# Performance work log

Hardware: AMD Instinct MI355X
Metric: run time of the kernel (lower is better)

Reference implementation:

```python
import jax, jax.numpy as jnp
import numpy as np

MASKED = True


def setup_inputs() -> dict:
    key = jax.random.key(0)
    kq, kk, kv = jax.random.split(key, 3)
    shape = (4, 16, 2048, 64)  # [B, H, S, d]
    q = jax.random.normal(kq, shape, dtype=jnp.float32)
    k = jax.random.normal(kk, shape, dtype=jnp.float32)
    v = jax.random.normal(kv, shape, dtype=jnp.float32)
    return {"q": q, "k": k, "v": v}


def reference(q, k, v):
    d = k.shape[-1]
    scale = 1.0 / jnp.sqrt(jnp.asarray(d, dtype=q.dtype))
    # [B, H, S, S]
    att = jnp.einsum("bhqd,bhkd->bhqk", q, k) * scale
    if MASKED:
        # Faithful to torch source: tril of the scores, then mask where zero
        tri = jnp.tril(att)
        att = jnp.where(tri == 0, -jnp.inf, att)
    att = jax.nn.softmax(att, axis=-1)
    return jnp.einsum("bhqk,bhkd->bhqd", att, v)
```

## Files before the change

kernel.cpp:

```cpp
#include <hip/hip_runtime.h>
#include <hip/hip_bf16.h>

typedef __attribute__((ext_vector_type(8)))  short bf16x8;
typedef __attribute__((ext_vector_type(4)))  float f32x4;
typedef __attribute__((ext_vector_type(16))) float f32x16;
typedef unsigned short ushort_t;

#define S_LEN 2048
#define D_DIM 64

#if __has_builtin(__builtin_amdgcn_exp2f)
#define EXP2(x) __builtin_amdgcn_exp2f(x)
#else
#define EXP2(x) __expf((x) * 0.6931471805599453f)
#endif

__device__ __forceinline__ short f2bf(float f) {
  union { float f; unsigned u; } x; x.f = f;
  unsigned r = x.u + 0x7fffu + ((x.u >> 16) & 1u);
  return (short)(r >> 16);
}

__device__ __forceinline__ unsigned cvtpk_bf16(float lo, float hi) {
  unsigned r;
  asm("v_cvt_pk_bf16_f32 %0, %1, %2" : "=v"(r) : "v"(lo), "v"(hi));
  return r;
}

__device__ __forceinline__ void pl32swap(unsigned& a, unsigned& b) {
  asm volatile("v_permlane32_swap_b32 %0, %1" : "+v"(a), "+v"(b));
}

__device__ __forceinline__ void gl_lds16(const ushort_t* g, ushort_t* l) {
  __builtin_amdgcn_global_load_lds(
      (const __attribute__((address_space(1))) unsigned*)g,
      (__attribute__((address_space(3))) unsigned*)l, 16, 0, 0);
}

__global__ void conv_bf16_kernel(const float* __restrict__ in,
                                 ushort_t* __restrict__ out, long n8) {
  long i = (long)blockIdx.x * blockDim.x + threadIdx.x;
  const long stride = (long)gridDim.x * blockDim.x;
  for (; i < n8; i += stride) {
    const float4* p = (const float4*)(in + i * 8);
    float4 a = p[0], b = p[1];
    bf16x8 t;
    t[0]=f2bf(a.x); t[1]=f2bf(a.y); t[2]=f2bf(a.z); t[3]=f2bf(a.w);
    t[4]=f2bf(b.x); t[5]=f2bf(b.y); t[6]=f2bf(b.z); t[7]=f2bf(b.w);
    *(bf16x8*)(out + i * 8) = t;
  }
}

__global__ void transpose_v_kernel(const float* __restrict__ V,
                                   ushort_t* __restrict__ Vt) {
  const int h  = blockIdx.x >> 5;
  const int s0 = (blockIdx.x & 31) * 64;
  const float* Vh = V + (size_t)h * S_LEN * D_DIM;
  ushort_t* Vth   = Vt + (size_t)h * D_DIM * S_LEN;
  __shared__ float tile[64][65];
  const int r  = threadIdx.x >> 2;
  const int c4 = (threadIdx.x & 3) * 16;
#pragma unroll
  for (int j = 0; j < 16; j += 4) {
    float4 x = *(const float4*)(Vh + (size_t)(s0 + r) * D_DIM + c4 + j);
    tile[r][c4 + j + 0] = x.x; tile[r][c4 + j + 1] = x.y;
    tile[r][c4 + j + 2] = x.z; tile[r][c4 + j + 3] = x.w;
  }
  __syncthreads();
  bf16x8 o0, o1;
#pragma unroll
  for (int j = 0; j < 8; ++j) o0[j] = f2bf(tile[c4 + j][r]);
#pragma unroll
  for (int j = 0; j < 8; ++j) o1[j] = f2bf(tile[c4 + 8 + j][r]);
  *(bf16x8*)(Vth + (size_t)r * S_LEN + s0 + c4)     = o0;
  *(bf16x8*)(Vth + (size_t)r * S_LEN + s0 + c4 + 8) = o1;
}

__global__ __launch_bounds__(256, 4)
void flash32_kernel(const float* __restrict__ Qf, const ushort_t* __restrict__ Kb,
                    const ushort_t* __restrict__ Vt, float* __restrict__ Og) {
  const int tid = threadIdx.x;
  const int l   = tid & 63;
  const int wv  = tid >> 6;
  const int hi  = l >> 5;
  const int l31 = l & 31;
  const int l7  = l & 7;
  const int l8  = l >> 3;

  const int qperm[16] = {15,14,13,12, 0,1,2,3, 11,10,9,8, 4,5,6,7};
  const int bid  = blockIdx.x;
  const int head = bid & 63;
  const int qidx = qperm[bid >> 6];
  const int q0   = qidx * 128;
  const int nt   = 2 * qidx + 2;

  const float*    Qh = Qf + (size_t)head * S_LEN * D_DIM;
  const ushort_t* Kh = Kb + (size_t)head * S_LEN * D_DIM;
  const ushort_t* Vh = Vt + (size_t)head * D_DIM * S_LEN;
  float*          Oh = Og + (size_t)head * S_LEN * D_DIM;

  __shared__ ushort_t smK[2][64 * 64];
  __shared__ ushort_t smV[2][64 * 64];

  const int qrow  = q0 + wv * 32 + l31;
  const int qminw = q0 + wv * 32;
  const int qmaxw = qminw + 31;

  const int swsrc = (l7 ^ l8) * 8;

#define STAGE(T, B) do {                                                   \
    const int kv_ = (T) * 64;                                              \
    _Pragma("unroll")                                                      \
    for (int u_ = 0; u_ < 4; ++u_) {                                       \
      const int idx_ = wv * 4 + u_;                                        \
      if (idx_ < 8) {                                                      \
        const int row_ = idx_ * 8 + l8;                                    \
        gl_lds16(Kh + (size_t)(kv_ + row_) * 64 + swsrc,                   \
                 &smK[B][idx_ * 512]);                                     \
      } else {                                                             \
        const int d_ = (idx_ - 8) * 8 + l8;                                \
        gl_lds16(Vh + (size_t)d_ * S_LEN + kv_ + swsrc,                    \
                 &smV[B][(idx_ - 8) * 512]);                               \
      }                                                                    \
    }                                                                      \
  } while (0)

  STAGE(0, 0);

  bf16x8 qf[4];
  {
    const float sc = 0.125f * 1.44269504089f;
    const float* qp = Qh + (size_t)qrow * D_DIM + 8 * hi;
#pragma unroll
    for (int ks = 0; ks < 4; ++ks) {
      float4 x = *(const float4*)(qp + ks * 16);
      float4 y = *(const float4*)(qp + ks * 16 + 4);
      bf16x8 t;
      t[0]=f2bf(x.x*sc); t[1]=f2bf(x.y*sc);
      t[2]=f2bf(x.z*sc); t[3]=f2bf(x.w*sc);
      t[4]=f2bf(y.x*sc); t[5]=f2bf(y.y*sc);
      t[6]=f2bf(y.z*sc); t[7]=f2bf(y.w*sc);
      qf[ks] = t;
    }
  }

  f32x16 accA, accB;
#pragma unroll
  for (int i = 0; i < 16; ++i) { accA[i] = 0.f; accB[i] = 0.f; }
  float m_run = -1e30f, l_run = 0.f;

  for (int t = 0; t < nt; ++t) {
    const int kv0 = t * 64;
    if (t + 1 < nt) {
      STAGE(t + 1, (t + 1) & 1);
      asm volatile("s_waitcnt vmcnt(4)" ::: "memory");
    } else {
      asm volatile("s_waitcnt vmcnt(0)" ::: "memory");
    }
    __builtin_amdgcn_s_barrier();
    __builtin_amdgcn_sched_barrier(0);

    if (kv0 <= qmaxw) {
      const ushort_t* kb = smK[t & 1];
      const ushort_t* vb = smV[t & 1];
      const int rb = l31 * 64;

      f32x16 s0, s1;
#pragma unroll
      for (int i = 0; i < 16; ++i) { s0[i] = 0.f; s1[i] = 0.f; }
      __builtin_amdgcn_s_setprio(1);
#pragma unroll
      for (int ks = 0; ks < 4; ++ks) {
        const int ch = ((ks * 2 + hi) ^ l7) * 8;
        bf16x8 a0 = *(const bf16x8*)(kb + rb + ch);
        bf16x8 a1 = *(const bf16x8*)(kb + 2048 + rb + ch);
        s0 = __builtin_amdgcn_mfma_f32_32x32x16_bf16(a0, qf[ks], s0, 0, 0, 0);
        s1 = __builtin_amdgcn_mfma_f32_32x32x16_bf16(a1, qf[ks], s1, 0, 0, 0);
      }
      __builtin_amdgcn_s_setprio(0);

      if (kv0 + 63 > qminw) {
#pragma unroll
        for (int r = 0; r < 16; ++r) {
          const int crow = (r & 3) + 8 * (r >> 2) + 4 * hi;
          if (kv0 + crow > qrow)      s0[r] = -INFINITY;
          if (kv0 + 32 + crow > qrow) s1[r] = -INFINITY;
        }
      }

      float a8[8];
#pragma unroll
      for (int i = 0; i < 8; ++i)
        a8[i] = fmaxf(fmaxf(s0[i], s0[i + 8]), fmaxf(s1[i], s1[i + 8]));
#pragma unroll
      for (int i = 0; i < 4; ++i) a8[i] = fmaxf(a8[i], a8[i + 4]);
      float mx = fmaxf(fmaxf(a8[0], a8[2]), fmaxf(a8[1], a8[3]));
      mx = fmaxf(mx, __shfl_xor(mx, 32, 64));

      if (!__all(mx - m_run <= 11.0f)) {
        const float mn    = fmaxf(m_run, mx);
        const float alpha = EXP2(m_run - mn);
        m_run = mn;
        l_run *= alpha;
        accA *= alpha;
        accB *= alpha;
      }

#pragma unroll
      for (int i = 0; i < 16; ++i) s0[i] = EXP2(s0[i] - m_run);
#pragma unroll
      for (int i = 0; i < 16; ++i) s1[i] = EXP2(s1[i] - m_run);
      float b8[8];
#pragma unroll
      for (int i = 0; i < 8; ++i)
        b8[i] = (s0[i] + s0[i + 8]) + (s1[i] + s1[i + 8]);
#pragma unroll
      for (int i = 0; i < 4; ++i) b8[i] += b8[i + 4];
      float sum = (b8[0] + b8[2]) + (b8[1] + b8[3]);
      sum += __shfl_xor(sum, 32, 64);
      l_run += sum;

      bf16x8 pw[4];
#pragma unroll
      for (int ks = 0; ks < 4; ++ks) {
        const int r0 = (ks & 1) * 8;
        unsigned w0, w1, w2, w3;
        if (ks < 2) {
          w0 = cvtpk_bf16(s0[r0+0], s0[r0+1]); w2 = cvtpk_bf16(s0[r0+4], s0[r0+5]);
          w1 = cvtpk_bf16(s0[r0+2], s0[r0+3]); w3 = cvtpk_bf16(s0[r0+6], s0[r0+7]);
        } else {
          w0 = cvtpk_bf16(s1[r0+0], s1[r0+1]); w2 = cvtpk_bf16(s1[r0+4], s1[r0+5]);
          w1 = cvtpk_bf16(s1[r0+2], s1[r0+3]); w3 = cvtpk_bf16(s1[r0+6], s1[r0+7]);
        }
        pl32swap(w0, w2);
        pl32swap(w1, w3);
        union { unsigned u[4]; bf16x8 v; } pu;
        pu.u[0] = w0; pu.u[1] = w1; pu.u[2] = w2; pu.u[3] = w3;
        pw[ks] = pu.v;
      }

      __builtin_amdgcn_s_setprio(1);
#pragma unroll
      for (int ks = 0; ks < 4; ++ks) {
        const int ch = ((ks * 2 + hi) ^ l7) * 8;
        bf16x8 va = *(const bf16x8*)(vb + rb + ch);
        bf16x8 vB = *(const bf16x8*)(vb + 2048 + rb + ch);
        accA = __builtin_amdgcn_mfma_f32_32x32x16_bf16(va, pw[ks], accA, 0, 0, 0);
        accB = __builtin_amdgcn_mfma_f32_32x32x16_bf16(vB, pw[ks], accB, 0, 0, 0);
      }
      __builtin_amdgcn_s_setprio(0);
    }
    __builtin_amdgcn_s_barrier();
  }
#undef STAGE

  const float inv = 1.0f / l_run;
  float* op = Oh + (size_t)qrow * D_DIM + 4 * hi;
#pragma unroll
  for (int m4 = 0; m4 < 4; ++m4) {
    float4 a = { accA[4*m4+0]*inv, accA[4*m4+1]*inv,
                 accA[4*m4+2]*inv, accA[4*m4+3]*inv };
    *(float4*)(op + 8 * m4) = a;
    float4 b = { accB[4*m4+0]*inv, accB[4*m4+1]*inv,
                 accB[4*m4+2]*inv, accB[4*m4+3]*inv };
    *(float4*)(op + 32 + 8 * m4) = b;
  }
}

#define BQ 64
#define BK 64
#define LDK 72
#define LDP 72

__device__ __forceinline__ unsigned pack_bf(float lo, float hi) {
  return (unsigned)(unsigned short)f2bf(lo) |
         ((unsigned)(unsigned short)f2bf(hi) << 16);
}

__global__ __launch_bounds__(256, 2)
void flash_fwd_kernel(const float* __restrict__ Qg, const float* __restrict__ Kg,
                      const float* __restrict__ Vg, float* __restrict__ Og) {
  const int tid  = threadIdx.x;
  const int lane = tid & 63;
  const int wv   = tid >> 6;
  const int grp  = lane >> 4;
  const int l16  = lane & 15;
  const int bid = blockIdx.x;
  const int qb  = 31 - (bid & 31);
  const int bh  = bid >> 5;
  const int q0  = qb * BQ;
  const size_t hoff = (size_t)bh * S_LEN * D_DIM;
  const float* Qh = Qg + hoff;
  const float* Kh = Kg + hoff;
  const float* Vh = Vg + hoff;
  float*       Oh = Og + hoff;
  __shared__ short sK [BK][LDK];
  __shared__ short sVT[D_DIM][LDP];
  __shared__ short sP [4][16][LDP];
  bf16x8 qf[2];
  {
    const float* qrow = Qh + (size_t)(q0 + wv*16 + l16) * D_DIM + grp*8;
#pragma unroll
    for (int kc = 0; kc < 2; ++kc) {
      float4 a = *reinterpret_cast<const float4*>(qrow + kc*32);
      float4 b = *reinterpret_cast<const float4*>(qrow + kc*32 + 4);
      bf16x8 t;
      t[0]=f2bf(a.x*0.125f); t[1]=f2bf(a.y*0.125f);
      t[2]=f2bf(a.z*0.125f); t[3]=f2bf(a.w*0.125f);
      t[4]=f2bf(b.x*0.125f); t[5]=f2bf(b.y*0.125f);
      t[6]=f2bf(b.z*0.125f); t[7]=f2bf(b.w*0.125f);
      qf[kc] = t;
    }
  }
  f32x4 acc[4];
#pragma unroll
  for (int nb = 0; nb < 4; ++nb) acc[nb] = (f32x4){0.f, 0.f, 0.f, 0.f};
  float m_i[4] = {-INFINITY, -INFINITY, -INFINITY, -INFINITY};
  float l_i[4] = {0.f, 0.f, 0.f, 0.f};
  const int srow = tid >> 2;
  const int scb  = tid & 3;
  for (int kt = 0; kt <= qb; ++kt) {
    const int kv0 = kt * BK;
    __syncthreads();
    {
      const float* src = Kh + (size_t)(kv0 + srow) * D_DIM + scb*16;
      float4 x0 = *reinterpret_cast<const float4*>(src);
      float4 x1 = *reinterpret_cast<const float4*>(src + 4);
      float4 x2 = *reinterpret_cast<const float4*>(src + 8);
      float4 x3 = *reinterpret_cast<const float4*>(src + 12);
      bf16x8 lo, hi;
      lo[0]=f2bf(x0.x); lo[1]=f2bf(x0.y); lo[2]=f2bf(x0.z); lo[3]=f2bf(x0.w);
      lo[4]=f2bf(x1.x); lo[5]=f2bf(x1.y); lo[6]=f2bf(x1.z); lo[7]=f2bf(x1.w);
      hi[0]=f2bf(x2.x); hi[1]=f2bf(x2.y); hi[2]=f2bf(x2.z); hi[3]=f2bf(x2.w);
      hi[4]=f2bf(x3.x); hi[5]=f2bf(x3.y); hi[6]=f2bf(x3.z); hi[7]=f2bf(x3.w);
      *reinterpret_cast<bf16x8*>(&sK[srow][scb*16])     = lo;
      *reinterpret_cast<bf16x8*>(&sK[srow][scb*16 + 8]) = hi;
    }
    {
      const float* src = Vh + (size_t)(kv0 + scb*16) * D_DIM + srow;
      bf16x8 lo, hi;
#pragma unroll
      for (int j = 0; j < 8; ++j) lo[j] = f2bf(src[(size_t)j * D_DIM]);
#pragma unroll
      for (int j = 0; j < 8; ++j) hi[j] = f2bf(src[(size_t)(j + 8) * D_DIM]);
      *reinterpret_cast<bf16x8*>(&sVT[srow][scb*16])     = lo;
      *reinterpret_cast<bf16x8*>(&sVT[srow][scb*16 + 8]) = hi;
    }
    __syncthreads();
    f32x4 sc[4];
#pragma unroll
    for (int nb = 0; nb < 4; ++nb) {
      f32x4 c = (f32x4){0.f, 0.f, 0.f, 0.f};
#pragma unroll
      for (int kc = 0; kc < 2; ++kc) {
        bf16x8 kf = *reinterpret_cast<const bf16x8*>(&sK[nb*16 + l16][kc*32 + grp*8]);
        c = __builtin_amdgcn_mfma_f32_16x16x32_bf16(qf[kc], kf, c, 0, 0, 0);
      }
      sc[nb] = c;
    }
    const bool diag = (kt == qb);
#pragma unroll
    for (int r = 0; r < 4; ++r) {
      const int qi = wv*16 + grp*4 + r;
      float s0 = sc[0][r], s1 = sc[1][r], s2 = sc[2][r], s3 = sc[3][r];
      if (diag) {
        if (l16 +  0 > qi) s0 = -INFINITY;
        if (l16 + 16 > qi) s1 = -INFINITY;
        if (l16 + 32 > qi) s2 = -INFINITY;
        if (l16 + 48 > qi) s3 = -INFINITY;
      }
      float mx = fmaxf(fmaxf(s0, s1), fmaxf(s2, s3));
#pragma unroll
      for (int off = 8; off; off >>= 1)
        mx = fmaxf(mx, __shfl_xor(mx, off, 64));
      const float mn    = fmaxf(m_i[r], mx);
      const float alpha = __expf(m_i[r] - mn);
      const float p0 = __expf(s0 - mn);
      const float p1 = __expf(s1 - mn);
      const float p2 = __expf(s2 - mn);
      const float p3 = __expf(s3 - mn);
      float rs = (p0 + p1) + (p2 + p3);
#pragma unroll
      for (int off = 8; off; off >>= 1)
        rs += __shfl_xor(rs, off, 64);
      l_i[r] = l_i[r] * alpha + rs;
      m_i[r] = mn;
      acc[0][r] *= alpha; acc[1][r] *= alpha;
      acc[2][r] *= alpha; acc[3][r] *= alpha;
      const float n0 = __shfl_xor(p0, 1, 64);
      const float n1 = __shfl_xor(p1, 1, 64);
      const float n2 = __shfl_xor(p2, 1, 64);
      const float n3 = __shfl_xor(p3, 1, 64);
      if (!(lane & 1)) {
        const int prow = grp*4 + r;
        unsigned* base = reinterpret_cast<unsigned*>(&sP[wv][prow][l16]);
        base[0]  = pack_bf(p0, n0);
        base[8]  = pack_bf(p1, n1);
        base[16] = pack_bf(p2, n2);
        base[24] = pack_bf(p3, n3);
      }
    }
    bf16x8 pf[2];
#pragma unroll
    for (int kc = 0; kc < 2; ++kc)
      pf[kc] = *reinterpret_cast<const bf16x8*>(&sP[wv][l16][kc*32 + grp*8]);
#pragma unroll
    for (int nb = 0; nb < 4; ++nb) {
#pragma unroll
      for (int kc = 0; kc < 2; ++kc) {
        bf16x8 vf = *reinterpret_cast<const bf16x8*>(&sVT[l16 + 16*nb][kc*32 + grp*8]);
        acc[nb] = __builtin_amdgcn_mfma_f32_16x16x32_bf16(pf[kc], vf, acc[nb], 0, 0, 0);
      }
    }
  }
#pragma unroll
  for (int r = 0; r < 4; ++r) {
    const float inv = 1.0f / l_i[r];
    float* orow = Oh + (size_t)(q0 + wv*16 + grp*4 + r) * D_DIM + l16;
#pragma unroll
    for (int nb = 0; nb < 4; ++nb)
      orow[nb*16] = acc[nb][r] * inv;
  }
}

extern "C" void kernel_launch(void* const* d_in, const int* in_sizes, int n_in,
                              void* d_out, int out_size, void* d_ws, size_t ws_size,
                              hipStream_t stream) {
  (void)n_in; (void)out_size;
  const float* q = (const float*)d_in[0];
  const float* k = (const float*)d_in[1];
  const float* v = (const float*)d_in[2];
  float* o = (float*)d_out;
  const int bh = in_sizes[0] / (S_LEN * D_DIM);
  const size_t elems = (size_t)bh * S_LEN * D_DIM;

  if (ws_size >= elems * 2 * 2) {
    ushort_t* Kb = (ushort_t*)d_ws;
    ushort_t* Vt = Kb + elems;
    const long n8 = (long)(elems / 8);
    conv_bf16_kernel<<<2048, 256, 0, stream>>>(k, Kb, n8);
    transpose_v_kernel<<<bh * (S_LEN / 64), 256, 0, stream>>>(v, Vt);
    flash32_kernel<<<bh * (S_LEN / 128), 256, 0, stream>>>(q, Kb, Vt, o);
  } else {
    flash_fwd_kernel<<<bh * (S_LEN / BQ), 256, 0, stream>>>(q, k, v, o);
  }
}
```

Measured before the change: 82.70 us.

## Software-pipeline QK^T of next tile with softmax and PV of current tile

Restructures the flash-attention main loop into a two-stage software pipeline: K and V loads are staged separately, and the QK^T MFMAs for tile t+1 are issued before the softmax and PV of tile t, unrolled by two with ping-pong score registers. This is meant to overlap matrix-core work with the exp/max/sum vector work and the global-to-LDS loads. It holds twice as many score accumulators, so launch bounds drop from 4 to 3 blocks per CU, which lowers occupancy. The per-wave skip of fully masked tiles (kv0 > qmaxw) is removed, so waves now also compute tiles that are entirely masked.

```diff
diff --git a/kernel.cpp b/kernel.cpp
--- a/kernel.cpp
+++ b/kernel.cpp
@@ -76,7 +76,7 @@
   *(bf16x8*)(Vth + (size_t)r * S_LEN + s0 + c4 + 8) = o1;
 }
 
-__global__ __launch_bounds__(256, 4)
+__global__ __launch_bounds__(256, 3)
 void flash32_kernel(const float* __restrict__ Qf, const ushort_t* __restrict__ Kb,
                     const ushort_t* __restrict__ Vt, float* __restrict__ Og) {
   const int tid = threadIdx.x;
@@ -104,28 +104,120 @@
 
   const int qrow  = q0 + wv * 32 + l31;
   const int qminw = q0 + wv * 32;
-  const int qmaxw = qminw + 31;
 
   const int swsrc = (l7 ^ l8) * 8;
-
-#define STAGE(T, B) do {                                                   \
-    const int kv_ = (T) * 64;                                              \
-    _Pragma("unroll")                                                      \
-    for (int u_ = 0; u_ < 4; ++u_) {                                       \
-      const int idx_ = wv * 4 + u_;                                        \
-      if (idx_ < 8) {                                                      \
-        const int row_ = idx_ * 8 + l8;                                    \
-        gl_lds16(Kh + (size_t)(kv_ + row_) * 64 + swsrc,                   \
-                 &smK[B][idx_ * 512]);                                     \
+  const int rb    = l31 * 64;
+
+#define STAGE_K(T, B) do {                                                 \
+    const int kvk_ = (T) * 64;                                             \
+    _Pragma("unroll")                                                      \
+    for (int u_ = 0; u_ < 2; ++u_) {                                       \
+      const int idx_ = wv * 2 + u_;                                        \
+      const int row_ = idx_ * 8 + l8;                                      \
+      gl_lds16(Kh + (size_t)(kvk_ + row_) * 64 + swsrc,                    \
+               &smK[B][idx_ * 512]);                                       \
+    }                                                                      \
+  } while (0)
+
+#define STAGE_V(T, B) do {                                                 \
+    const int kvv_ = (T) * 64;                                             \
+    _Pragma("unroll")                                                      \
+    for (int u_ = 0; u_ < 2; ++u_) {                                       \
+      const int idx_ = wv * 2 + u_;                                        \
+      const int d_ = idx_ * 8 + l8;                                        \
+      gl_lds16(Vh + (size_t)d_ * S_LEN + kvv_ + swsrc,                     \
+               &smV[B][idx_ * 512]);                                       \
+    }                                                                      \
+  } while (0)
+
+#define VMCNT(N) asm volatile("s_waitcnt vmcnt(" #N ")" ::: "memory")
+
+#define QKT(S0, S1, KB) do {                                               \
+    _Pragma("unroll")                                                      \
+    for (int i = 0; i < 16; ++i) { S0[i] = 0.f; S1[i] = 0.f; }             \
+    const ushort_t* kb_ = smK[KB];                                         \
+    __builtin_amdgcn_s_setprio(1);                                         \
+    _Pragma("unroll")                                                      \
+    for (int ks = 0; ks < 4; ++ks) {                                       \
+      const int ch = ((ks * 2 + hi) ^ l7) * 8;                             \
+      bf16x8 a0 = *(const bf16x8*)(kb_ + rb + ch);                         \
+      bf16x8 a1 = *(const bf16x8*)(kb_ + 2048 + rb + ch);                  \
+      S0 = __builtin_amdgcn_mfma_f32_32x32x16_bf16(a0, qf[ks], S0, 0, 0, 0); \
+      S1 = __builtin_amdgcn_mfma_f32_32x32x16_bf16(a1, qf[ks], S1, 0, 0, 0); \
+    }                                                                      \
+    __builtin_amdgcn_s_setprio(0);                                         \
+  } while (0)
+
+#define SOFTMAX(S0, S1, KV0) do {                                          \
+    if ((KV0) + 63 > qminw) {                                              \
+      _Pragma("unroll")                                                    \
+      for (int r = 0; r < 16; ++r) {                                       \
+        const int crow = (r & 3) + 8 * (r >> 2) + 4 * hi;                  \
+        if ((KV0) + crow > qrow)      S0[r] = -INFINITY;                   \
+        if ((KV0) + 32 + crow > qrow) S1[r] = -INFINITY;                   \
+      }                                                                    \
+    }                                                                      \
+    float a8[8];                                                           \
+    _Pragma("unroll")                                                      \
+    for (int i = 0; i < 8; ++i)                                            \
+      a8[i] = fmaxf(fmaxf(S0[i], S0[i+8]), fmaxf(S1[i], S1[i+8]));         \
+    _Pragma("unroll")                                                      \
+    for (int i = 0; i < 4; ++i) a8[i] = fmaxf(a8[i], a8[i+4]);             \
+    float mx = fmaxf(fmaxf(a8[0], a8[2]), fmaxf(a8[1], a8[3]));            \
+    mx = fmaxf(mx, __shfl_xor(mx, 32, 64));                                \
+    if (!__all(mx - m_run <= 11.0f)) {            \
+      const float mn    = fmaxf(m_run, mx);                                \
+      const float alpha = EXP2(m_run - mn);                                \
+      m_run = mn; l_run *= alpha; accA *= alpha; accB *= alpha;            \
+    }                                                                      \
+    _Pragma("unroll")                                                      \
+    for (int i = 0; i < 16; ++i) S0[i] = EXP2(S0[i] - m_run);              \
+    _Pragma("unroll")                                                      \
+    for (int i = 0; i < 16; ++i) S1[i] = EXP2(S1[i] - m_run);              \
+    float b8[8];                                                           \
+    _Pragma("unroll")                                                      \
+    for (int i = 0; i < 8; ++i)                                            \
+      b8[i] = (S0[i] + S0[i+8]) + (S1[i] + S1[i+8]);                       \
+    _Pragma("unroll")                                                      \
+    for (int i = 0; i < 4; ++i) b8[i] += b8[i+4];                          \
+    float sum = (b8[0] + b8[2]) + (b8[1] + b8[3]);                         \
+    sum += __shfl_xor(sum, 32, 64);                                        \
+    l_run += sum;                                                          \
+    _Pragma("unroll")                                                      \
+    for (int ks = 0; ks < 4; ++ks) {                                       \
+      const int r0 = (ks & 1) * 8;                                         \
+      unsigned w0, w1, w2, w3;                                             \
+      if (ks < 2) {                                                        \
+        w0 = cvtpk_bf16(S0[r0+0], S0[r0+1]); w2 = cvtpk_bf16(S0[r0+4], S0[r0+5]); \
+        w1 = cvtpk_bf16(S0[r0+2], S0[r0+3]); w3 = cvtpk_bf16(S0[r0+6], S0[r0+7]); \
       } else {                                                             \
-        const int d_ = (idx_ - 8) * 8 + l8;                                \
-        gl_lds16(Vh + (size_t)d_ * S_LEN + kv_ + swsrc,                    \
-                 &smV[B][(idx_ - 8) * 512]);                               \
+        w0 = cvtpk_bf16(S1[r0+0], S1[r0+1]); w2 = cvtpk_bf16(S1[r0+4], S1[r0+5]); \
+        w1 = cvtpk_bf16(S1[r0+2], S1[r0+3]); w3 = cvtpk_bf16(S1[r0+6], S1[r0+7]); \
       }                                                                    \
+      pl32swap(w0, w2); pl32swap(w1, w3);                                  \
+      union { unsigned u[4]; bf16x8 v; } pu_;                              \
+      pu_.u[0] = w0; pu_.u[1] = w1; pu_.u[2] = w2; pu_.u[3] = w3;          \
+      pw[ks] = pu_.v;                                                      \
     }                                                                      \
   } while (0)
 
-  STAGE(0, 0);
+#define PV(VB) do {                                                        \
+    const ushort_t* vb_ = smV[VB];                                         \
+    __builtin_amdgcn_s_setprio(1);                                         \
+    _Pragma("unroll")                                                      \
+    for (int ks = 0; ks < 4; ++ks) {                                       \
+      const int ch = ((ks * 2 + hi) ^ l7) * 8;                             \
+      bf16x8 va = *(const bf16x8*)(vb_ + rb + ch);                         \
+      bf16x8 vB2 = *(const bf16x8*)(vb_ + 2048 + rb + ch);                 \
+      accA = __builtin_amdgcn_mfma_f32_32x32x16_bf16(va,  pw[ks], accA, 0, 0, 0); \
+      accB = __builtin_amdgcn_mfma_f32_32x32x16_bf16(vB2, pw[ks], accB, 0, 0, 0); \
+    }                                                                      \
+    __builtin_amdgcn_s_setprio(0);                                         \
+  } while (0)
+
+  STAGE_K(0, 0);
+  STAGE_V(0, 0);
+  STAGE_K(1, 1);
 
   bf16x8 qf[4];
   {
@@ -144,115 +236,50 @@
     }
   }
 
-  f32x16 accA, accB;
+  f32x16 accA, accB, sA0, sA1, sB0, sB1;
 #pragma unroll
   for (int i = 0; i < 16; ++i) { accA[i] = 0.f; accB[i] = 0.f; }
   float m_run = -1e30f, l_run = 0.f;
-
-  for (int t = 0; t < nt; ++t) {
-    const int kv0 = t * 64;
-    if (t + 1 < nt) {
-      STAGE(t + 1, (t + 1) & 1);
-      asm volatile("s_waitcnt vmcnt(4)" ::: "memory");
-    } else {
-      asm volatile("s_waitcnt vmcnt(0)" ::: "memory");
-    }
+  bf16x8 pw[4];
+
+  VMCNT(4);
+  __builtin_amdgcn_s_barrier();
+  QKT(sA0, sA1, 0);
+
+  for (int t = 0; t + 2 < nt; t += 2) {
     __builtin_amdgcn_s_barrier();
-    __builtin_amdgcn_sched_barrier(0);
-
-    if (kv0 <= qmaxw) {
-      const ushort_t* kb = smK[t & 1];
-      const ushort_t* vb = smV[t & 1];
-      const int rb = l31 * 64;
-
-      f32x16 s0, s1;
-#pragma unroll
-      for (int i = 0; i < 16; ++i) { s0[i] = 0.f; s1[i] = 0.f; }
-      __builtin_amdgcn_s_setprio(1);
-#pragma unroll
-      for (int ks = 0; ks < 4; ++ks) {
-        const int ch = ((ks * 2 + hi) ^ l7) * 8;
-        bf16x8 a0 = *(const bf16x8*)(kb + rb + ch);
-        bf16x8 a1 = *(const bf16x8*)(kb + 2048 + rb + ch);
-        s0 = __builtin_amdgcn_mfma_f32_32x32x16_bf16(a0, qf[ks], s0, 0, 0, 0);
-        s1 = __builtin_amdgcn_mfma_f32_32x32x16_bf16(a1, qf[ks], s1, 0, 0, 0);
-      }
-      __builtin_amdgcn_s_setprio(0);
-
-      if (kv0 + 63 > qminw) {
-#pragma unroll
-        for (int r = 0; r < 16; ++r) {
-          const int crow = (r & 3) + 8 * (r >> 2) + 4 * hi;
-          if (kv0 + crow > qrow)      s0[r] = -INFINITY;
-          if (kv0 + 32 + crow > qrow) s1[r] = -INFINITY;
-        }
-      }
-
-      float a8[8];
-#pragma unroll
-      for (int i = 0; i < 8; ++i)
-        a8[i] = fmaxf(fmaxf(s0[i], s0[i + 8]), fmaxf(s1[i], s1[i + 8]));
-#pragma unroll
-      for (int i = 0; i < 4; ++i) a8[i] = fmaxf(a8[i], a8[i + 4]);
-      float mx = fmaxf(fmaxf(a8[0], a8[2]), fmaxf(a8[1], a8[3]));
-      mx = fmaxf(mx, __shfl_xor(mx, 32, 64));
-
-      if (!__all(mx - m_run <= 11.0f)) {
-        const float mn    = fmaxf(m_run, mx);
-        const float alpha = EXP2(m_run - mn);
-        m_run = mn;
-        l_run *= alpha;
-        accA *= alpha;
-        accB *= alpha;
-      }
-
-#pragma unroll
-      for (int i = 0; i < 16; ++i) s0[i] = EXP2(s0[i] - m_run);
-#pragma unroll
-      for (int i = 0; i < 16; ++i) s1[i] = EXP2(s1[i] - m_run);
-      float b8[8];
-#pragma unroll
-      for (int i = 0; i < 8; ++i)
-        b8[i] = (s0[i] + s0[i + 8]) + (s1[i] + s1[i + 8]);
-#pragma unroll
-      for (int i = 0; i < 4; ++i) b8[i] += b8[i + 4];
-      float sum = (b8[0] + b8[2]) + (b8[1] + b8[3]);
-      sum += __shfl_xor(sum, 32, 64);
-      l_run += sum;
-
-      bf16x8 pw[4];
-#pragma unroll
-      for (int ks = 0; ks < 4; ++ks) {
-        const int r0 = (ks & 1) * 8;
-        unsigned w0, w1, w2, w3;
-        if (ks < 2) {
-          w0 = cvtpk_bf16(s0[r0+0], s0[r0+1]); w2 = cvtpk_bf16(s0[r0+4], s0[r0+5]);
-          w1 = cvtpk_bf16(s0[r0+2], s0[r0+3]); w3 = cvtpk_bf16(s0[r0+6], s0[r0+7]);
-        } else {
-          w0 = cvtpk_bf16(s1[r0+0], s1[r0+1]); w2 = cvtpk_bf16(s1[r0+4], s1[r0+5]);
-          w1 = cvtpk_bf16(s1[r0+2], s1[r0+3]); w3 = cvtpk_bf16(s1[r0+6], s1[r0+7]);
-        }
-        pl32swap(w0, w2);
-        pl32swap(w1, w3);
-        union { unsigned u[4]; bf16x8 v; } pu;
-        pu.u[0] = w0; pu.u[1] = w1; pu.u[2] = w2; pu.u[3] = w3;
-        pw[ks] = pu.v;
-      }
-
-      __builtin_amdgcn_s_setprio(1);
-#pragma unroll
-      for (int ks = 0; ks < 4; ++ks) {
-        const int ch = ((ks * 2 + hi) ^ l7) * 8;
-        bf16x8 va = *(const bf16x8*)(vb + rb + ch);
-        bf16x8 vB = *(const bf16x8*)(vb + 2048 + rb + ch);
-        accA = __builtin_amdgcn_mfma_f32_32x32x16_bf16(va, pw[ks], accA, 0, 0, 0);
-        accB = __builtin_amdgcn_mfma_f32_32x32x16_bf16(vB, pw[ks], accB, 0, 0, 0);
-      }
-      __builtin_amdgcn_s_setprio(0);
-    }
+    STAGE_K(t + 2, 0);
+    STAGE_V(t + 1, 1);
+    VMCNT(4);
+    QKT(sB0, sB1, 1);
+    SOFTMAX(sA0, sA1, t * 64);
+    PV(0);
     __builtin_amdgcn_s_barrier();
-  }
-#undef STAGE
+    STAGE_K(t + 3, 1);
+    STAGE_V(t + 2, 0);
+    VMCNT(4);
+    QKT(sA0, sA1, 0);
+    SOFTMAX(sB0, sB1, (t + 1) * 64);
+    PV(1);
+  }
+
+  __builtin_amdgcn_s_barrier();
+  STAGE_V(nt - 1, 1);
+  VMCNT(2);
+  QKT(sB0, sB1, 1);
+  SOFTMAX(sA0, sA1, (nt - 2) * 64);
+  PV(0);
+  __builtin_amdgcn_s_barrier();
+  VMCNT(0);
+  SOFTMAX(sB0, sB1, (nt - 1) * 64);
+  PV(1);
+
+#undef STAGE_K
+#undef STAGE_V
+#undef VMCNT
+#undef QKT
+#undef SOFTMAX
+#undef PV
 
   const float inv = 1.0f / l_run;
   float* op = Oh + (size_t)qrow * D_DIM + 4 * hi;
```

New measurement: 79.63 us. 1.04x faster.
